# Optimization experiments

Measured on AMD Instinct MI355X. Metric: run time of the kernel, lower is better.

## Reference

```python
import jax, jax.numpy as jnp
import numpy as np

D_MODEL = 1024
NUM_HEADS = 16
D_K = D_MODEL // NUM_HEADS
TEMPERATURE = 1.0
EPS = 1e-6


def setup_inputs() -> dict:
    key = jax.random.key(0)
    ks = jax.random.split(key, 8)
    B, S, D, H = 2, 2048, D_MODEL, NUM_HEADS
    sc = 1.0 / np.sqrt(D)
    x = jax.random.normal(ks[0], (B, S, D), dtype=jnp.float32)
    Wq = jax.random.normal(ks[1], (D, D), dtype=jnp.float32) * sc
    Wk = jax.random.normal(ks[2], (D, D), dtype=jnp.float32) * sc
    Wv = jax.random.normal(ks[3], (D, D), dtype=jnp.float32) * sc
    Wo = jax.random.normal(ks[4], (D, D), dtype=jnp.float32) * sc
    bo = jnp.zeros((D,), dtype=jnp.float32)
    phase_scale = jnp.ones((H,), dtype=jnp.float32)
    # orthogonal init for entanglement matrix
    q, _ = np.linalg.qr(np.random.default_rng(0).normal(size=(H, H)))
    ent = jnp.asarray(q, dtype=jnp.float32)
    gamma = jnp.ones((D,), dtype=jnp.float32)
    beta = jnp.zeros((D,), dtype=jnp.float32)
    return {"x": x, "Wq": Wq, "Wk": Wk, "Wv": Wv, "Wo": Wo, "bo": bo,
            "phase_scale": phase_scale, "ent": ent, "gamma": gamma, "beta": beta}


def reference(x, Wq, Wk, Wv, Wo, bo, phase_scale, ent, gamma, beta):
    B, S, D = x.shape
    H, dk = NUM_HEADS, D_K
    # projections -> [B, H, S, dk]
    Q = (x @ Wq).reshape(B, S, H, dk).transpose(0, 2, 1, 3)
    K = (x @ Wk).reshape(B, S, H, dk).transpose(0, 2, 1, 3)
    V = (x @ Wv).reshape(B, S, H, dk).transpose(0, 2, 1, 3)
    # per-head QK^T, scaled, phase-modulated
    scores = jnp.einsum('bhqd,bhkd->bhqk', Q, K)
    inv = 1.0 / (float(np.sqrt(dk)) * TEMPERATURE)
    s = scores * (inv * phase_scale)[None, :, None, None]
    # real part of quantum phase: cos(s) + 0.1*cos(2s)  (imag part of V is zero,
    # so head_output = attended_real; the 0.1*attended_imag term vanishes)
    w = jnp.cos(s) + 0.1 * jnp.cos(2.0 * s)
    w = jax.nn.softmax(w, axis=-1)
    att = jnp.einsum('bhqk,bhkd->bhqd', w, V).transpose(0, 2, 1, 3)  # [B,S,H,dk]
    # faithful reproduction of tf.einsum('bsnd,hm->bsmd', ...): sums over n AND h
    att = jnp.einsum('bsnd,hm->bsmd', att, ent)
    out = att.reshape(B, S, D) @ Wo + bo
    r = out + x
    mu = jnp.mean(r, axis=-1, keepdims=True)
    var = jnp.mean(jnp.square(r - mu), axis=-1, keepdims=True)
    return gamma * (r - mu) * jax.lax.rsqrt(var + EPS) + beta
```

## Files before the change

kernel.cpp:

```cpp
#include <hip/hip_runtime.h>
#include <cstdint>
#include <cstddef>

#define S_LEN 2048
#define DMODEL 1024
#define NHEADS 16
#define DKH 64
#define MROWS 4096
#define BH_CNT 32

typedef __bf16 bf16x8 __attribute__((ext_vector_type(8)));
typedef __bf16 bf16x2 __attribute__((ext_vector_type(2)));
typedef float f32x4 __attribute__((ext_vector_type(4)));
typedef unsigned int u32x4 __attribute__((ext_vector_type(4)));
typedef unsigned int u32;
typedef unsigned short u16;

__device__ __forceinline__ u16 f2bfu(float f) {
  u32 u = __float_as_uint(f);
  return (u16)((u + 0x7FFFu + ((u >> 16) & 1u)) >> 16);
}

__device__ __forceinline__ u32 pk_bf16(float a, float b) {
  bf16x2 v;
  v[0] = (__bf16)a;
  v[1] = (__bf16)b;
  return __builtin_bit_cast(u32, v);
}

__device__ __forceinline__ void pl32swap(u32& a, u32& b) {
#if __has_builtin(__builtin_amdgcn_permlane32_swap)
  auto r = __builtin_amdgcn_permlane32_swap((int)a, (int)b, false, false);
  a = (u32)r[0]; b = (u32)r[1];
#else
  asm volatile("v_permlane32_swap_b32 %0, %1" : "+v"(a), "+v"(b));
#endif
}
__device__ __forceinline__ void pl16swap(u32& a, u32& b) {
#if __has_builtin(__builtin_amdgcn_permlane16_swap)
  auto r = __builtin_amdgcn_permlane16_swap((int)a, (int)b, false, false);
  a = (u32)r[0]; b = (u32)r[1];
#else
  asm volatile("v_permlane16_swap_b32 %0, %1" : "+v"(a), "+v"(b));
#endif
}

__device__ __forceinline__ void gload16(void* lds, const void* g) {
  __builtin_amdgcn_global_load_lds(
      (const __attribute__((address_space(1))) void*)g,
      (__attribute__((address_space(3))) void*)lds, 16, 0, 0);
}

__global__ __launch_bounds__(256) void prep_xb_k(const float* __restrict__ x,
                                                 u16* __restrict__ xb) {
  int i = (blockIdx.x * 256 + threadIdx.x) * 4;
  float4 v = *(const float4*)(x + i);
  *(uint2*)(xb + i) = make_uint2(pk_bf16(v.x, v.y), pk_bf16(v.z, v.w));
}

__global__ __launch_bounds__(256) void prep_w_k(const float* __restrict__ Wq,
    const float* __restrict__ Wk, const float* __restrict__ Wv,
    const float* __restrict__ ps, u16* __restrict__ Wb) {
  __shared__ float tile[32][33];
  int sel = blockIdx.z;
  const float* W = sel == 0 ? Wq : (sel == 1 ? Wk : Wv);
  int k0 = blockIdx.x * 32, c0 = blockIdx.y * 32;
  int tx = threadIdx.x, ty = threadIdx.y;
#pragma unroll
  for (int i = 0; i < 4; ++i)
    tile[ty + i * 8][tx] = W[(size_t)(k0 + ty + i * 8) * DMODEL + c0 + tx];
  __syncthreads();
#pragma unroll
  for (int i = 0; i < 4; ++i) {
    int row = ty + i * 8;
    float v = tile[tx][row];
    if (sel == 1) v *= 0.019894367886486918f * ps[(c0 + row) >> 6];
    Wb[(size_t)(sel * 1024 + c0 + row) * DMODEL + k0 + tx] = f2bfu(v);
  }
}

__global__ __launch_bounds__(256) void prep_woeff_k(const float* __restrict__ Wo,
    const float* __restrict__ ent, float* __restrict__ Woeff) {
  __shared__ float e[16];
  int t = threadIdx.x;
  if (t < 16) {
    float s = 0.f;
#pragma unroll
    for (int h = 0; h < 16; ++h) s += ent[h * 16 + t];
    e[t] = s;
  }
  __syncthreads();
  int gid = blockIdx.x * 256 + t;
  int d = gid >> 10, j = gid & 1023;
  float acc = 0.f;
#pragma unroll
  for (int m = 0; m < 16; ++m) acc += e[m] * Wo[(size_t)((m << 6) + d) * DMODEL + j];
  Woeff[(size_t)d * DMODEL + j] = acc;
}

__global__ __launch_bounds__(256) void gemm_qkv_k(const u16* __restrict__ xb,
    const u16* __restrict__ Wb, u16* __restrict__ Qb, u16* __restrict__ Kb,
    u16* __restrict__ Vt) {
  __shared__ __align__(16) u16 SMEM[2][2][128 * 32];
  int tid = threadIdx.x;
  int lane = tid & 63, w = tid >> 6;
  int c = lane & 15, g = lane >> 4;
  int wr = w >> 1, wc = w & 1;
  int m0 = blockIdx.x * 128, n0 = blockIdx.y * 128;

  int cij0 = (w * 2) * 64 + lane, cij1 = (w * 2 + 1) * 64 + lane;
  int row0 = cij0 >> 2, kp0 = (cij0 & 3) ^ (row0 & 3);
  int row1 = cij1 >> 2, kp1 = (cij1 & 3) ^ (row1 & 3);
  const u16* a0p = xb + (size_t)(m0 + row0) * DMODEL + kp0 * 8;
  const u16* a1p = xb + (size_t)(m0 + row1) * DMODEL + kp1 * 8;
  const u16* b0p = Wb + (size_t)(n0 + row0) * DMODEL + kp0 * 8;
  const u16* b1p = Wb + (size_t)(n0 + row1) * DMODEL + kp1 * 8;

  f32x4 acc[4][4];
#pragma unroll
  for (int i = 0; i < 4; ++i)
#pragma unroll
    for (int j = 0; j < 4; ++j) acc[i][j] = (f32x4){0.f, 0.f, 0.f, 0.f};

  gload16(&SMEM[0][0][(w * 2) * 512], a0p);
  gload16(&SMEM[0][0][(w * 2 + 1) * 512], a1p);
  gload16(&SMEM[1][0][(w * 2) * 512], b0p);
  gload16(&SMEM[1][0][(w * 2 + 1) * 512], b1p);
  __syncthreads();

  int cur = 0;
  for (int kt = 0; kt < DMODEL; kt += 32) {
    if (kt + 32 < DMODEL) {
      int nx = cur ^ 1, ko = kt + 32;
      gload16(&SMEM[0][nx][(w * 2) * 512], a0p + ko);
      gload16(&SMEM[0][nx][(w * 2 + 1) * 512], a1p + ko);
      gload16(&SMEM[1][nx][(w * 2) * 512], b0p + ko);
      gload16(&SMEM[1][nx][(w * 2 + 1) * 512], b1p + ko);
    }
    const u16* Ac = SMEM[0][cur];
    const u16* Bc = SMEM[1][cur];
    bf16x8 af[4], bf[4];
#pragma unroll
    for (int i = 0; i < 4; ++i) {
      int ra = wr * 64 + i * 16 + c;
      af[i] = *(const bf16x8*)(Ac + ra * 32 + ((g ^ (ra & 3)) * 8));
      int rb = wc * 64 + i * 16 + c;
      bf[i] = *(const bf16x8*)(Bc + rb * 32 + ((g ^ (rb & 3)) * 8));
    }
#pragma unroll
    for (int i = 0; i < 4; ++i)
#pragma unroll
      for (int j = 0; j < 4; ++j)
        acc[i][j] = __builtin_amdgcn_mfma_f32_16x16x32_bf16(af[i], bf[j], acc[i][j], 0, 0, 0);
    __syncthreads();
    cur ^= 1;
  }

  int sel = n0 >> 10;
  char* Ls = (char*)&SMEM[0][0][0];
  if (sel == 2) {
#pragma unroll
    for (int i = 0; i < 4; ++i)
#pragma unroll
      for (int jf = 0; jf < 4; ++jf) {
        int n = wc * 64 + jf * 16 + c;
        int m = wr * 64 + i * 16 + 4 * g;
        int byte = n * 256 + ((m * 2) ^ ((n & 7) << 4));
        *(uint2*)(Ls + byte) = make_uint2(pk_bf16(acc[i][jf][0], acc[i][jf][1]),
                                          pk_bf16(acc[i][jf][2], acc[i][jf][3]));
      }
  } else {
#pragma unroll
    for (int i = 0; i < 4; ++i)
#pragma unroll
      for (int jf = 0; jf < 4; ++jf) {
        int n = wc * 64 + jf * 16 + c;
#pragma unroll
        for (int j = 0; j < 4; ++j) {
          int m = wr * 64 + i * 16 + 4 * g + j;
          int byte = m * 256 + ((n * 2) ^ ((m & 7) << 4));
          __bf16 hv = (__bf16)acc[i][jf][j];
          *(u16*)(Ls + byte) = __builtin_bit_cast(u16, hv);
        }
      }
  }
  __syncthreads();
  int r = tid >> 1, half = tid & 1;
  int h0 = (n0 & 1023) >> 6;
  int b = m0 >> 11, sbase = m0 & 2047;
  u16* dst;
  if (sel == 2) {
    int bh = b * 16 + h0 + (r >> 6), d = r & 63;
    dst = Vt + ((size_t)bh * DKH + d) * S_LEN + sbase + half * 64;
  } else {
    u16* base = (sel == 0 ? Qb : Kb);
    int bh = b * 16 + h0 + half;
    dst = base + ((size_t)bh * S_LEN + sbase + r) * DKH;
  }
#pragma unroll
  for (int kk = 0; kk < 8; ++kk) {
    int byte = r * 256 + ((half * 128 + kk * 16) ^ ((r & 7) << 4));
    *(uint4*)(dst + kk * 8) = *(const uint4*)(Ls + byte);
  }
}

__global__ __launch_bounds__(256) void attn_k(const u16* __restrict__ Qb,
    const u16* __restrict__ Kb, const u16* __restrict__ Vt,
    float* __restrict__ attbuf) {
  __shared__ __align__(16) u16 Ks[2][64 * 64];
  __shared__ __align__(16) u16 Vs[2][64 * 64];
  __shared__ float dred[4][2][16];
  int fid = blockIdx.x;
  int swz = (fid & 7) * 128 + (fid >> 3);
  int bh = swz >> 5, qblk = swz & 31;
  int tid = threadIdx.x;
  int lane = tid & 63, w = tid >> 6;
  int c = lane & 15, g = lane >> 4;
  int h = w >> 1, qh = w & 1;
  int q0 = qblk * 64;
  const u16* Kbase = Kb + (size_t)bh * S_LEN * DKH;
  const u16* Vbase = Vt + (size_t)bh * DKH * S_LEN;

  int cij0 = (w * 2) * 64 + lane, cij1 = (w * 2 + 1) * 64 + lane;
  int srow0 = cij0 >> 3, skp0 = (cij0 & 7) ^ (srow0 & 7);
  int srow1 = cij1 >> 3, skp1 = (cij1 & 7) ^ (srow1 & 7);
  const u16* k0p = Kbase + (size_t)srow0 * DKH + skp0 * 8;
  const u16* k1p = Kbase + (size_t)srow1 * DKH + skp1 * 8;
  const u16* v0p = Vbase + (size_t)srow0 * S_LEN + skp0 * 8;
  const u16* v1p = Vbase + (size_t)srow1 * S_LEN + skp1 * 8;

  gload16(&Ks[0][(w * 2) * 512], k0p);
  gload16(&Ks[0][(w * 2 + 1) * 512], k1p);
  gload16(&Vs[0][(w * 2) * 512], v0p);
  gload16(&Vs[0][(w * 2 + 1) * 512], v1p);

  bf16x8 qf[2][2];
#pragma unroll
  for (int qg = 0; qg < 2; ++qg) {
    const u16* qp = Qb + ((size_t)bh * S_LEN + q0 + qh * 32 + qg * 16 + c) * DKH + g * 8;
    qf[qg][0] = *(const bf16x8*)qp;
    qf[qg][1] = *(const bf16x8*)(qp + 32);
  }
  f32x4 attT[4][2];
#pragma unroll
  for (int i = 0; i < 4; ++i)
#pragma unroll
    for (int qg = 0; qg < 2; ++qg) attT[i][qg] = (f32x4){0.f, 0.f, 0.f, 0.f};
  float dacc[2] = {0.f, 0.f};
  const float L2E = 1.4426950408889634f;

  auto compute = [&](const u16* Kc, const u16* Vc) {
    f32x4 sT[2][2];
    __builtin_amdgcn_s_setprio(1);
#pragma unroll
    for (int fm = 0; fm < 2; ++fm) {
      int row = h * 32 + fm * 16 + c;
      bf16x8 a0 = *(const bf16x8*)(Kc + row * 64 + ((g ^ (row & 7)) * 8));
      bf16x8 a1 = *(const bf16x8*)(Kc + row * 64 + (((4 + g) ^ (row & 7)) * 8));
#pragma unroll
      for (int qg = 0; qg < 2; ++qg) {
        f32x4 z = (f32x4){0.f, 0.f, 0.f, 0.f};
        z = __builtin_amdgcn_mfma_f32_16x16x32_bf16(a0, qf[qg][0], z, 0, 0, 0);
        sT[fm][qg] = __builtin_amdgcn_mfma_f32_16x16x32_bf16(a1, qf[qg][1], z, 0, 0, 0);
      }
    }
    __builtin_amdgcn_s_setprio(0);
    u32 wq[2][2][2];
#pragma unroll
    for (int fm = 0; fm < 2; ++fm)
#pragma unroll
      for (int qg = 0; qg < 2; ++qg) {
        float pv[4];
#pragma unroll
        for (int j = 0; j < 4; ++j) {
          float cv = __builtin_amdgcn_cosf(sT[fm][qg][j]);
          float w2 = __fmaf_rn(cv, __fmaf_rn(0.2f * L2E, cv, L2E), -0.1f * L2E);
          pv[j] = __builtin_amdgcn_exp2f(w2);
        }
        dacc[qg] += (pv[0] + pv[1]) + (pv[2] + pv[3]);
        wq[qg][fm][0] = pk_bf16(pv[0], pv[1]);
        wq[qg][fm][1] = pk_bf16(pv[2], pv[3]);
      }
    bf16x8 pf[2];
#pragma unroll
    for (int qg = 0; qg < 2; ++qg) {
      u32 b0 = wq[qg][0][0], b2 = wq[qg][1][0];
      pl32swap(b0, b2);
      pl16swap(b0, b2);
      u32 b1 = wq[qg][0][1], b3 = wq[qg][1][1];
      pl32swap(b1, b3);
      pl16swap(b1, b3);
      pf[qg] = __builtin_bit_cast(bf16x8, (u32x4){b0, b1, b2, b3});
    }
    __builtin_amdgcn_s_setprio(1);
#pragma unroll
    for (int fd = 0; fd < 4; ++fd) {
      int vrow = fd * 16 + c;
      bf16x8 vf = *(const bf16x8*)(Vc + vrow * 64 + (((4 * h + g) ^ (vrow & 7)) * 8));
#pragma unroll
      for (int qg = 0; qg < 2; ++qg)
        attT[fd][qg] = __builtin_amdgcn_mfma_f32_16x16x32_bf16(vf, pf[qg], attT[fd][qg], 0, 0, 0);
    }
    __builtin_amdgcn_s_setprio(0);
  };

  const u16* kc0 = k0p;
  const u16* kc1 = k1p;
  const u16* vc0 = v0p;
  const u16* vc1 = v1p;
  __syncthreads();
  for (int kt = 0; kt < S_LEN; kt += 128) {
    kc0 += 64 * DKH; kc1 += 64 * DKH; vc0 += 64; vc1 += 64;
    gload16(&Ks[1][(w * 2) * 512], kc0);
    gload16(&Ks[1][(w * 2 + 1) * 512], kc1);
    gload16(&Vs[1][(w * 2) * 512], vc0);
    gload16(&Vs[1][(w * 2 + 1) * 512], vc1);
    compute(Ks[0], Vs[0]);
    __syncthreads();
    if (kt + 128 < S_LEN) {
      kc0 += 64 * DKH; kc1 += 64 * DKH; vc0 += 64; vc1 += 64;
      gload16(&Ks[0][(w * 2) * 512], kc0);
      gload16(&Ks[0][(w * 2 + 1) * 512], kc1);
      gload16(&Vs[0][(w * 2) * 512], vc0);
      gload16(&Vs[0][(w * 2 + 1) * 512], vc1);
    }
    compute(Ks[1], Vs[1]);
    __syncthreads();
  }

#pragma unroll
  for (int qg = 0; qg < 2; ++qg) {
    dacc[qg] += __shfl_xor(dacc[qg], 16, 64);
    dacc[qg] += __shfl_xor(dacc[qg], 32, 64);
  }
  if (g == 0) {
    dred[w][0][c] = dacc[0];
    dred[w][1][c] = dacc[1];
  }
  float* R = (float*)&Ks[0][0];
  if (h == 1) {
    float* Rq = R + qh * 2048;
#pragma unroll
    for (int fd = 0; fd < 4; ++fd)
#pragma unroll
      for (int qg = 0; qg < 2; ++qg)
        *(f32x4*)&Rq[(qg * 16 + c) * 64 + fd * 16 + 4 * g] = attT[fd][qg];
  }
  __syncthreads();
  if (h == 0) {
    float inv[2];
#pragma unroll
    for (int qg = 0; qg < 2; ++qg)
      inv[qg] = 1.f / (dred[w][qg][c] + dred[w ^ 2][qg][c]);
    float* Rq = R + qh * 2048;
#pragma unroll
    for (int fd = 0; fd < 4; ++fd)
#pragma unroll
      for (int qg = 0; qg < 2; ++qg) {
        f32x4 part = *(const f32x4*)&Rq[(qg * 16 + c) * 64 + fd * 16 + 4 * g];
        f32x4 tot = (attT[fd][qg] + part) * inv[qg];
        int q = q0 + qh * 32 + qg * 16 + c;
        *(f32x4*)(attbuf + ((size_t)bh * S_LEN + q) * DKH + fd * 16 + 4 * g) = tot;
      }
  }
}

__global__ __launch_bounds__(256) void fuse_out_ln_k(const float* __restrict__ attbuf,
    const float* __restrict__ Woeff, const float* __restrict__ bo,
    const float* __restrict__ x, const float* __restrict__ gamma,
    const float* __restrict__ beta, float* __restrict__ out) {
  __shared__ float red[8][256];
  __shared__ __align__(16) float a[8][64];
  __shared__ float sred[8][4][2];
  int t = threadIdx.x;
  int r0 = blockIdx.x * 8;
  int d = t & 63, hg = t >> 6;
#pragma unroll
  for (int rr = 0; rr < 8; ++rr) {
    int m = r0 + rr, b = m >> 11, sr = m & 2047;
    float pa = 0.f;
#pragma unroll
    for (int hh = 0; hh < 4; ++hh) {
      int h = hg * 4 + hh;
      pa += attbuf[(((size_t)(b * 16 + h)) * S_LEN + sr) * DKH + d];
    }
    red[rr][t] = pa;
  }
  __syncthreads();
#pragma unroll
  for (int e = 0; e < 2; ++e) {
    int idx = t + e * 256;
    int rr = idx >> 6, dd = idx & 63;
    a[rr][dd] = red[rr][dd] + red[rr][64 + dd] + red[rr][128 + dd] + red[rr][192 + dd];
  }
  __syncthreads();

  float o[8][4];
#pragma unroll
  for (int rr = 0; rr < 8; ++rr) { o[rr][0] = o[rr][1] = o[rr][2] = o[rr][3] = 0.f; }
  int c4 = t * 4;
  for (int dd = 0; dd < 64; dd += 4) {
    float4 wv0 = *(const float4*)(Woeff + (size_t)(dd + 0) * DMODEL + c4);
    float4 wv1 = *(const float4*)(Woeff + (size_t)(dd + 1) * DMODEL + c4);
    float4 wv2 = *(const float4*)(Woeff + (size_t)(dd + 2) * DMODEL + c4);
    float4 wv3 = *(const float4*)(Woeff + (size_t)(dd + 3) * DMODEL + c4);
#pragma unroll
    for (int rr = 0; rr < 8; ++rr) {
      float4 av = *(const float4*)&a[rr][dd];
      o[rr][0] += av.x * wv0.x + av.y * wv1.x + av.z * wv2.x + av.w * wv3.x;
      o[rr][1] += av.x * wv0.y + av.y * wv1.y + av.z * wv2.y + av.w * wv3.y;
      o[rr][2] += av.x * wv0.z + av.y * wv1.z + av.z * wv2.z + av.w * wv3.z;
      o[rr][3] += av.x * wv0.w + av.y * wv1.w + av.z * wv2.w + av.w * wv3.w;
    }
  }
  float4 bv = *(const float4*)(bo + c4);
  int w = t >> 6, lane = t & 63;
#pragma unroll
  for (int rr = 0; rr < 8; ++rr) {
    int m = r0 + rr;
    float4 xv = *(const float4*)(x + (size_t)m * DMODEL + c4);
    o[rr][0] += bv.x + xv.x;
    o[rr][1] += bv.y + xv.y;
    o[rr][2] += bv.z + xv.z;
    o[rr][3] += bv.w + xv.w;
    float s = o[rr][0] + o[rr][1] + o[rr][2] + o[rr][3];
    float q = o[rr][0] * o[rr][0] + o[rr][1] * o[rr][1] + o[rr][2] * o[rr][2] + o[rr][3] * o[rr][3];
#pragma unroll
    for (int mm = 1; mm < 64; mm <<= 1) {
      s += __shfl_xor(s, mm, 64);
      q += __shfl_xor(q, mm, 64);
    }
    if (lane == 0) { sred[rr][w][0] = s; sred[rr][w][1] = q; }
  }
  __syncthreads();
  float4 gv = *(const float4*)(gamma + c4);
  float4 bev = *(const float4*)(beta + c4);
#pragma unroll
  for (int rr = 0; rr < 8; ++rr) {
    float s = sred[rr][0][0] + sred[rr][1][0] + sred[rr][2][0] + sred[rr][3][0];
    float q = sred[rr][0][1] + sred[rr][1][1] + sred[rr][2][1] + sred[rr][3][1];
    float mu = s * (1.f / 1024.f);
    float var = q * (1.f / 1024.f) - mu * mu;
    float rs = rsqrtf(var + 1e-6f);
    int m = r0 + rr;
    float4 ov;
    ov.x = gv.x * (o[rr][0] - mu) * rs + bev.x;
    ov.y = gv.y * (o[rr][1] - mu) * rs + bev.y;
    ov.z = gv.z * (o[rr][2] - mu) * rs + bev.z;
    ov.w = gv.w * (o[rr][3] - mu) * rs + bev.w;
    *(float4*)(out + (size_t)m * DMODEL + c4) = ov;
  }
}

extern "C" void kernel_launch(void* const* d_in, const int* in_sizes, int n_in,
                              void* d_out, int out_size, void* d_ws, size_t ws_size,
                              hipStream_t stream) {
  const float* x = (const float*)d_in[0];
  const float* Wq = (const float*)d_in[1];
  const float* Wk = (const float*)d_in[2];
  const float* Wv = (const float*)d_in[3];
  const float* Wo = (const float*)d_in[4];
  const float* bo = (const float*)d_in[5];
  const float* ps = (const float*)d_in[6];
  const float* ent = (const float*)d_in[7];
  const float* gamma = (const float*)d_in[8];
  const float* beta = (const float*)d_in[9];
  float* out = (float*)d_out;

  char* ws = (char*)d_ws;
  size_t o = 0;
  u16* xb = (u16*)(ws + o);    o += (size_t)MROWS * DMODEL * 2;
  u16* Wb = (u16*)(ws + o);    o += (size_t)3072 * 1024 * 2;
  u16* Qb = (u16*)(ws + o);    o += (size_t)BH_CNT * S_LEN * DKH * 2;
  u16* Kb = (u16*)(ws + o);    o += (size_t)BH_CNT * S_LEN * DKH * 2;
  u16* Vt = (u16*)(ws + o);    o += (size_t)BH_CNT * S_LEN * DKH * 2;
  float* Woeff = (float*)(ws + o);  o += (size_t)DKH * DMODEL * 4;
  float* attbuf = (float*)(ws + o); o += (size_t)BH_CNT * S_LEN * DKH * 4;

  prep_xb_k<<<dim3(4096), dim3(256), 0, stream>>>(x, xb);
  prep_w_k<<<dim3(32, 32, 3), dim3(32, 8), 0, stream>>>(Wq, Wk, Wv, ps, Wb);
  prep_woeff_k<<<dim3(256), dim3(256), 0, stream>>>(Wo, ent, Woeff);
  gemm_qkv_k<<<dim3(32, 24), dim3(256), 0, stream>>>(xb, Wb, Qb, Kb, Vt);
  attn_k<<<dim3(1024), dim3(256), 0, stream>>>(Qb, Kb, Vt, attbuf);
  fuse_out_ln_k<<<dim3(512), dim3(256), 0, stream>>>(attbuf, Woeff, bo, x, gamma, beta, out);
}
```

Baseline: 143.4 us.

## Replace attention cos/exp with LDS lookup table, MFMA row sums, XCD-aware GEMM tiling

The attention kernel now builds a 2048-entry bf16 table of exp(cos(2πu)+0.1cos(4πu)) in shared memory and looks it up by the fractional part of the score, replacing the per-element cos and exp2 transcendentals. Softmax denominators are accumulated by an extra MFMA against a ones vector instead of scalar adds and shuffles. K/V tiles are visited in a rotated order starting at the query block, and launch bounds request higher occupancy. The QKV GEMM switches to a 1D grid with XCD-aware tile remapping for better L2 locality. The LUT quantizes the phase to 2048 steps, which adds approximation error, and the extra shared memory and occupancy hint may raise register pressure.

```diff
diff --git a/kernel.cpp b/kernel.cpp
--- a/kernel.cpp
+++ b/kernel.cpp
@@ -102,11 +102,16 @@
     const u16* __restrict__ Wb, u16* __restrict__ Qb, u16* __restrict__ Kb,
     u16* __restrict__ Vt) {
   __shared__ __align__(16) u16 SMEM[2][2][128 * 32];
+  int bid = blockIdx.x;
+  int xcd = bid & 7, wi = bid >> 3;
+  int mg = xcd >> 1, ng = xcd & 1;
+  int mt = mg * 8 + (wi & 7);
+  int nt = ng * 12 + (wi >> 3);
+  int m0 = mt * 128, n0 = nt * 128;
   int tid = threadIdx.x;
   int lane = tid & 63, w = tid >> 6;
   int c = lane & 15, g = lane >> 4;
   int wr = w >> 1, wc = w & 1;
-  int m0 = blockIdx.x * 128, n0 = blockIdx.y * 128;
 
   int cij0 = (w * 2) * 64 + lane, cij1 = (w * 2 + 1) * 64 + lane;
   int row0 = cij0 >> 2, kp0 = (cij0 & 3) ^ (row0 & 3);
@@ -204,11 +209,12 @@
   }
 }
 
-__global__ __launch_bounds__(256) void attn_k(const u16* __restrict__ Qb,
+__global__ __launch_bounds__(256, 4) void attn_k(const u16* __restrict__ Qb,
     const u16* __restrict__ Kb, const u16* __restrict__ Vt,
     float* __restrict__ attbuf) {
   __shared__ __align__(16) u16 Ks[2][64 * 64];
   __shared__ __align__(16) u16 Vs[2][64 * 64];
+  __shared__ u16 Lut[2048];
   __shared__ float dred[4][2][16];
   int fid = blockIdx.x;
   int swz = (fid & 7) * 128 + (fid >> 3);
@@ -218,9 +224,19 @@
   int c = lane & 15, g = lane >> 4;
   int h = w >> 1, qh = w & 1;
   int q0 = qblk * 64;
+  const float L2E = 1.4426950408889634f;
+
+#pragma unroll
+  for (int e = 0; e < 8; ++e) {
+    int i = tid + e * 256;
+    float cv = __builtin_amdgcn_cosf((float)i * (1.f / 2048.f));
+    float w2 = __fmaf_rn(cv, __fmaf_rn(0.2f * L2E, cv, L2E), -0.1f * L2E);
+    __bf16 hv = (__bf16)__builtin_amdgcn_exp2f(w2);
+    Lut[i] = __builtin_bit_cast(u16, hv);
+  }
+
   const u16* Kbase = Kb + (size_t)bh * S_LEN * DKH;
   const u16* Vbase = Vt + (size_t)bh * DKH * S_LEN;
-
   int cij0 = (w * 2) * 64 + lane, cij1 = (w * 2 + 1) * 64 + lane;
   int srow0 = cij0 >> 3, skp0 = (cij0 & 7) ^ (srow0 & 7);
   int srow1 = cij1 >> 3, skp1 = (cij1 & 7) ^ (srow1 & 7);
@@ -229,10 +245,14 @@
   const u16* v0p = Vbase + (size_t)srow0 * S_LEN + skp0 * 8;
   const u16* v1p = Vbase + (size_t)srow1 * S_LEN + skp1 * 8;
 
-  gload16(&Ks[0][(w * 2) * 512], k0p);
-  gload16(&Ks[0][(w * 2 + 1) * 512], k1p);
-  gload16(&Vs[0][(w * 2) * 512], v0p);
-  gload16(&Vs[0][(w * 2 + 1) * 512], v1p);
+  auto stage = [&](int buf, int tile) {
+    gload16(&Ks[buf][(w * 2) * 512], k0p + (size_t)tile * 64 * DKH);
+    gload16(&Ks[buf][(w * 2 + 1) * 512], k1p + (size_t)tile * 64 * DKH);
+    gload16(&Vs[buf][(w * 2) * 512], v0p + tile * 64);
+    gload16(&Vs[buf][(w * 2 + 1) * 512], v1p + tile * 64);
+  };
+
+  stage(0, qblk);
 
   bf16x8 qf[2][2];
 #pragma unroll
@@ -241,13 +261,17 @@
     qf[qg][0] = *(const bf16x8*)qp;
     qf[qg][1] = *(const bf16x8*)(qp + 32);
   }
+  bf16x8 onesf;
+#pragma unroll
+  for (int i = 0; i < 8; ++i) onesf[i] = (__bf16)1.0f;
   f32x4 attT[4][2];
 #pragma unroll
   for (int i = 0; i < 4; ++i)
 #pragma unroll
     for (int qg = 0; qg < 2; ++qg) attT[i][qg] = (f32x4){0.f, 0.f, 0.f, 0.f};
-  float dacc[2] = {0.f, 0.f};
-  const float L2E = 1.4426950408889634f;
+  f32x4 denacc[2];
+  denacc[0] = (f32x4){0.f, 0.f, 0.f, 0.f};
+  denacc[1] = (f32x4){0.f, 0.f, 0.f, 0.f};
 
   auto compute = [&](const u16* Kc, const u16* Vc) {
     f32x4 sT[2][2];
@@ -270,16 +294,15 @@
     for (int fm = 0; fm < 2; ++fm)
 #pragma unroll
       for (int qg = 0; qg < 2; ++qg) {
-        float pv[4];
+        u32 pb[4];
 #pragma unroll
         for (int j = 0; j < 4; ++j) {
-          float cv = __builtin_amdgcn_cosf(sT[fm][qg][j]);
-          float w2 = __fmaf_rn(cv, __fmaf_rn(0.2f * L2E, cv, L2E), -0.1f * L2E);
-          pv[j] = __builtin_amdgcn_exp2f(w2);
+          float u = __builtin_amdgcn_fractf(sT[fm][qg][j]);
+          int idx = (int)__fmaf_rn(u, 2048.f, 0.5f) & 2047;
+          pb[j] = (u32)Lut[idx];
         }
-        dacc[qg] += (pv[0] + pv[1]) + (pv[2] + pv[3]);
-        wq[qg][fm][0] = pk_bf16(pv[0], pv[1]);
-        wq[qg][fm][1] = pk_bf16(pv[2], pv[3]);
+        wq[qg][fm][0] = pb[0] | (pb[1] << 16);
+        wq[qg][fm][1] = pb[2] | (pb[3] << 16);
       }
     bf16x8 pf[2];
 #pragma unroll
@@ -301,41 +324,25 @@
       for (int qg = 0; qg < 2; ++qg)
         attT[fd][qg] = __builtin_amdgcn_mfma_f32_16x16x32_bf16(vf, pf[qg], attT[fd][qg], 0, 0, 0);
     }
+#pragma unroll
+    for (int qg = 0; qg < 2; ++qg)
+      denacc[qg] = __builtin_amdgcn_mfma_f32_16x16x32_bf16(onesf, pf[qg], denacc[qg], 0, 0, 0);
     __builtin_amdgcn_s_setprio(0);
   };
 
-  const u16* kc0 = k0p;
-  const u16* kc1 = k1p;
-  const u16* vc0 = v0p;
-  const u16* vc1 = v1p;
-  __syncthreads();
-  for (int kt = 0; kt < S_LEN; kt += 128) {
-    kc0 += 64 * DKH; kc1 += 64 * DKH; vc0 += 64; vc1 += 64;
-    gload16(&Ks[1][(w * 2) * 512], kc0);
-    gload16(&Ks[1][(w * 2 + 1) * 512], kc1);
-    gload16(&Vs[1][(w * 2) * 512], vc0);
-    gload16(&Vs[1][(w * 2 + 1) * 512], vc1);
+  __syncthreads();
+  for (int t = 0; t < 32; t += 2) {
+    stage(1, (t + 1 + qblk) & 31);
     compute(Ks[0], Vs[0]);
     __syncthreads();
-    if (kt + 128 < S_LEN) {
-      kc0 += 64 * DKH; kc1 += 64 * DKH; vc0 += 64; vc1 += 64;
-      gload16(&Ks[0][(w * 2) * 512], kc0);
-      gload16(&Ks[0][(w * 2 + 1) * 512], kc1);
-      gload16(&Vs[0][(w * 2) * 512], vc0);
-      gload16(&Vs[0][(w * 2 + 1) * 512], vc1);
-    }
+    if (t + 2 < 32) stage(0, (t + 2 + qblk) & 31);
     compute(Ks[1], Vs[1]);
     __syncthreads();
   }
 
-#pragma unroll
-  for (int qg = 0; qg < 2; ++qg) {
-    dacc[qg] += __shfl_xor(dacc[qg], 16, 64);
-    dacc[qg] += __shfl_xor(dacc[qg], 32, 64);
-  }
   if (g == 0) {
-    dred[w][0][c] = dacc[0];
-    dred[w][1][c] = dacc[1];
+    dred[w][0][c] = denacc[0][0];
+    dred[w][1][c] = denacc[1][0];
   }
   float* R = (float*)&Ks[0][0];
   if (h == 1) {
@@ -480,7 +487,7 @@
   prep_xb_k<<<dim3(4096), dim3(256), 0, stream>>>(x, xb);
   prep_w_k<<<dim3(32, 32, 3), dim3(32, 8), 0, stream>>>(Wq, Wk, Wv, ps, Wb);
   prep_woeff_k<<<dim3(256), dim3(256), 0, stream>>>(Wo, ent, Woeff);
-  gemm_qkv_k<<<dim3(32, 24), dim3(256), 0, stream>>>(xb, Wb, Qb, Kb, Vt);
+  gemm_qkv_k<<<dim3(768), dim3(256), 0, stream>>>(xb, Wb, Qb, Kb, Vt);
   attn_k<<<dim3(1024), dim3(256), 0, stream>>>(Qb, Kb, Vt, attbuf);
   fuse_out_ln_k<<<dim3(512), dim3(256), 0, stream>>>(attbuf, Woeff, bo, x, gamma, beta, out);
 }
```

New measurement: 132.9 us. 1.08x faster.
